# Performance work log

Measured on AMD Instinct MI355X. Metric: run time of the kernel, lower is better.

## Reference

```python
import jax, jax.numpy as jnp
import numpy as np

N, D, G = 16384, 2048, 4096  # points, vocab_size (feature dim), num_groups


def setup_inputs() -> dict:
    key = jax.random.key(0)
    kx, ke = jax.random.split(key)
    x = jax.random.normal(kx, (N, D), dtype=jnp.float32)
    # trunc_normal_ init for the codebook; plain normal is fine for a numeric reference
    emb = jax.random.truncated_normal(ke, -2.0, 2.0, (G, D), dtype=jnp.float32)
    return {"x": x, "emb": emb}


def reference(x, emb):
    x2 = jnp.sum(x * x, axis=-1, keepdims=True)          # [N, 1]
    e2 = jnp.sum(emb * emb, axis=-1)                     # [G]
    sq = x2 + e2[None, :] - 2.0 * (x @ emb.T)            # [N, G]
    dist = jnp.sqrt(jnp.maximum(sq, 0.0))
    return -dist
```

## Files before the change

kernel.cpp:

```cpp
#include <hip/hip_runtime.h>
#include <hip/hip_bf16.h>

#define NPTS 16384
#define DIM  2048
#define NGRP 4096
#define BK   32
#define NT   (DIM / BK)

typedef __bf16 bf16x8 __attribute__((ext_vector_type(8)));
typedef unsigned short u16x8 __attribute__((ext_vector_type(8)));
typedef float f32x4 __attribute__((ext_vector_type(4)));

__device__ __forceinline__ unsigned short f2bf(float f) {
  union { float f; unsigned u; } v; v.f = f;
  unsigned u = v.u;
  return (unsigned short)((u + 0x7FFFu + ((u >> 16) & 1u)) >> 16);
}
__device__ __forceinline__ float bflo(unsigned u) { return __uint_as_float(u << 16); }
__device__ __forceinline__ float bfhi(unsigned u) { return __uint_as_float(u & 0xffff0000u); }

__device__ __forceinline__ void gload16(const void* g, void* lds) {
  __builtin_amdgcn_global_load_lds(
      (const __attribute__((address_space(1))) unsigned*)g,
      (__attribute__((address_space(3))) unsigned*)lds, 16, 0, 0);
}

__device__ __forceinline__ bool sniff_bf16(const void* X) {
  const int lane = threadIdx.x & 63;
  unsigned hb = (((const unsigned short*)X)[lane] >> 8) & 0x7Fu;
  unsigned long long m = __ballot(hb >= 0x3Bu && hb <= 0x41u);
  return __popcll(m) >= 48;
}

__global__ __launch_bounds__(256) void prep_all_kernel(
    const void* __restrict__ Xin, const void* __restrict__ Ein,
    unsigned short* __restrict__ Xbf, unsigned short* __restrict__ Ebf,
    float* __restrict__ x2, float* __restrict__ e2) {
  const int lane  = threadIdx.x & 63;
  const int wavei = threadIdx.x >> 6;
  const bool isbf = sniff_bf16(Xin);

  const int grow = blockIdx.x * 4 + wavei;
  const void* in; unsigned short* q; float* nrm; int row;
  if (grow < NPTS) { in = Xin; q = Xbf; nrm = x2; row = grow; }
  else             { in = Ein; q = Ebf; nrm = e2; row = grow - NPTS; }

  float s = 0.f;
  if (isbf) {
    const unsigned short* p = (const unsigned short*)in + (size_t)row * DIM;
#pragma unroll
    for (int it = 0; it < 4; ++it) {
      uint4 v = *(const uint4*)(p + it * 512 + lane * 8);
      float f;
      f = bflo(v.x); s += f * f;  f = bfhi(v.x); s += f * f;
      f = bflo(v.y); s += f * f;  f = bfhi(v.y); s += f * f;
      f = bflo(v.z); s += f * f;  f = bfhi(v.z); s += f * f;
      f = bflo(v.w); s += f * f;  f = bfhi(v.w); s += f * f;
    }
  } else {
    const float* p = (const float*)in + (size_t)row * DIM;
    unsigned short* qq = q + (size_t)row * DIM;
#pragma unroll
    for (int it = 0; it < 4; ++it) {
      float4 a = *(const float4*)(p + it * 512 + lane * 8);
      float4 b = *(const float4*)(p + it * 512 + lane * 8 + 4);
      s += a.x * a.x + a.y * a.y + a.z * a.z + a.w * a.w;
      s += b.x * b.x + b.y * b.y + b.z * b.z + b.w * b.w;
      u16x8 r;
      r[0] = f2bf(a.x); r[1] = f2bf(a.y); r[2] = f2bf(a.z); r[3] = f2bf(a.w);
      r[4] = f2bf(b.x); r[5] = f2bf(b.y); r[6] = f2bf(b.z); r[7] = f2bf(b.w);
      *(u16x8*)(qq + it * 512 + lane * 8) = r;
    }
  }
#pragma unroll
  for (int off = 32; off > 0; off >>= 1) s += __shfl_down(s, off, 64);
  if (lane == 0) nrm[row] = s;
}

#define A_OFF 0
#define B_OFF 8192

__global__ __launch_bounds__(512, 2) void gemm_8p_kernel(
    const void* __restrict__ Xin, const unsigned short* __restrict__ Xws,
    const void* __restrict__ Ein, const unsigned short* __restrict__ Ews,
    const float* __restrict__ x2, const float* __restrict__ e2,
    void* __restrict__ outv) {
  __shared__ __align__(16) unsigned short sbuf[4][16384];

  const int tid  = threadIdx.x;
  const int lane = tid & 63;
  const int wave = tid >> 6;
  const int wm   = wave >> 2;
  const int wn   = wave & 3;
  const int quad = lane >> 4;
  const int l16  = lane & 15;

  const bool isbf = sniff_bf16(Xin);
  const unsigned short* X = isbf ? (const unsigned short*)Xin : Xws;
  const unsigned short* E = isbf ? (const unsigned short*)Ein : Ews;

  const int rowBase = blockIdx.y * 256;
  const int colBase = blockIdx.x * 256;

  const int srow = tid >> 2;
  const int scol = (tid & 3) * 8;
  const size_t gA = (size_t)(rowBase + srow) * DIM + scol;
  const size_t gB = (size_t)(colBase + srow) * DIM + scol;
  const size_t HSTRIDE = (size_t)128 * DIM;

  const int aoff = (wm * 128 + l16) * 32 + quad * 8;
  const int boff = B_OFF + (wn * 64 + l16) * 32 + quad * 8;

  f32x4 zero = {0.f, 0.f, 0.f, 0.f};
  f32x4 acc[8][4];
#pragma unroll
  for (int mt = 0; mt < 8; ++mt)
#pragma unroll
    for (int nt = 0; nt < 4; ++nt) acc[mt][nt] = zero;

#define STAGE_A(t_) do { const size_t k_ = (size_t)(t_) * BK;                         \
    gload16(X + gA + k_,           &sbuf[(t_) & 3][A_OFF + wave * 512]);              \
    gload16(X + gA + HSTRIDE + k_, &sbuf[(t_) & 3][A_OFF + 4096 + wave * 512]);       \
  } while (0)
#define STAGE_B(t_) do { const size_t k_ = (size_t)(t_) * BK;                         \
    gload16(E + gB + k_,           &sbuf[(t_) & 3][B_OFF + wave * 512]);              \
    gload16(E + gB + HSTRIDE + k_, &sbuf[(t_) & 3][B_OFF + 4096 + wave * 512]);       \
  } while (0)

#define TILE(t_, DOSTAGE_, VM_) do {                                                  \
    asm volatile("s_waitcnt vmcnt(" #VM_ ")" ::: "memory");                           \
    __builtin_amdgcn_s_barrier();                                                     \
    __builtin_amdgcn_sched_barrier(0);                                                \
    const unsigned short* sb_ = sbuf[(t_) & 3];                                       \
    bf16x8 aL_[4], aH_[4], bF_[4];                                                    \
    _Pragma("unroll") for (int mt = 0; mt < 4; ++mt)                                  \
      aL_[mt] = *(const bf16x8*)(const void*)(sb_ + aoff + mt * 512);                 \
    _Pragma("unroll") for (int nt = 0; nt < 4; ++nt)                                  \
      bF_[nt] = *(const bf16x8*)(const void*)(sb_ + boff + nt * 512);                 \
    if (DOSTAGE_) STAGE_A((t_) + 3);                                                  \
    __builtin_amdgcn_s_setprio(1);                                                    \
    _Pragma("unroll") for (int mt = 0; mt < 4; ++mt)                                  \
      _Pragma("unroll") for (int nt = 0; nt < 4; ++nt)                                \
        acc[mt][nt] = __builtin_amdgcn_mfma_f32_16x16x32_bf16(aL_[mt], bF_[nt],       \
                                                              acc[mt][nt], 0, 0, 0);  \
    __builtin_amdgcn_s_setprio(0);                                                    \
    asm volatile("" ::: "memory");                                                    \
    __builtin_amdgcn_s_barrier();                                                     \
    __builtin_amdgcn_sched_barrier(0);                                                \
    _Pragma("unroll") for (int mt = 0; mt < 4; ++mt)                                  \
      aH_[mt] = *(const bf16x8*)(const void*)(sb_ + aoff + (mt + 4) * 512);           \
    if (DOSTAGE_) STAGE_B((t_) + 3);                                                  \
    __builtin_amdgcn_s_setprio(1);                                                    \
    _Pragma("unroll") for (int mt = 0; mt < 4; ++mt)                                  \
      _Pragma("unroll") for (int nt = 0; nt < 4; ++nt)                                \
        acc[mt + 4][nt] = __builtin_amdgcn_mfma_f32_16x16x32_bf16(aH_[mt], bF_[nt],   \
                                                              acc[mt + 4][nt], 0, 0, 0); \
    __builtin_amdgcn_s_setprio(0);                                                    \
    asm volatile("" ::: "memory");                                                    \
    __builtin_amdgcn_s_barrier();                                                     \
    __builtin_amdgcn_sched_barrier(0);                                                \
  } while (0)

  STAGE_A(0); STAGE_B(0);
  STAGE_A(1); STAGE_B(1);
  STAGE_A(2); STAGE_B(2);

  for (int t = 0; t < NT - 3; ++t) {
    TILE(t, true, 8);
  }
  TILE(NT - 3, false, 8);
  TILE(NT - 2, false, 4);
  TILE(NT - 1, false, 0);
#undef TILE
#undef STAGE_A
#undef STAGE_B

  float ec[4];
#pragma unroll
  for (int nt = 0; nt < 4; ++nt) ec[nt] = e2[colBase + wn * 64 + nt * 16 + l16];

  if (isbf) {
    unsigned short* out = (unsigned short*)outv;
#pragma unroll
    for (int mt = 0; mt < 8; ++mt)
#pragma unroll
      for (int r = 0; r < 4; ++r) {
        const int row = rowBase + wm * 128 + mt * 16 + quad * 4 + r;
        const float xr = x2[row];
#pragma unroll
        for (int nt = 0; nt < 4; ++nt) {
          const int col = colBase + wn * 64 + nt * 16 + l16;
          float sq = xr + ec[nt] - 2.0f * acc[mt][nt][r];
          sq = sq > 0.f ? sq : 0.f;
          out[(size_t)row * NGRP + col] = f2bf(-__builtin_sqrtf(sq));
        }
      }
  } else {
    float* out = (float*)outv;
#pragma unroll
    for (int mt = 0; mt < 8; ++mt)
#pragma unroll
      for (int r = 0; r < 4; ++r) {
        const int row = rowBase + wm * 128 + mt * 16 + quad * 4 + r;
        const float xr = x2[row];
#pragma unroll
        for (int nt = 0; nt < 4; ++nt) {
          const int col = colBase + wn * 64 + nt * 16 + l16;
          float sq = xr + ec[nt] - 2.0f * acc[mt][nt][r];
          sq = sq > 0.f ? sq : 0.f;
          out[(size_t)row * NGRP + col] = -__builtin_sqrtf(sq);
        }
      }
  }
}


__global__ void sniff_kernel(const unsigned short* __restrict__ X, int* __restrict__ flag) {
  if (threadIdx.x == 0 && blockIdx.x == 0) {
    int c = 0;
    for (int i = 0; i < 64; ++i) {
      unsigned b = (X[i] >> 8) & 0x7F;
      c += (b >= 0x3B && b <= 0x41) ? 1 : 0;
    }
    *flag = (c >= 48) ? 1 : 0;
  }
}

__global__ __launch_bounds__(256) void rownorm_kernel(const void* __restrict__ in,
                                                      float* __restrict__ out,
                                                      const int* __restrict__ flag) {
  const int wave = threadIdx.x >> 6;
  const int lane = threadIdx.x & 63;
  const int row  = blockIdx.x * 4 + wave;
  float s = 0.f;
  if (*flag) {
    const unsigned short* p = (const unsigned short*)in + (size_t)row * DIM;
#pragma unroll
    for (int it = 0; it < 4; ++it) {
      uint4 v = *(const uint4*)(p + it * 512 + lane * 8);
      float f;
      f = bflo(v.x); s += f * f;  f = bfhi(v.x); s += f * f;
      f = bflo(v.y); s += f * f;  f = bfhi(v.y); s += f * f;
      f = bflo(v.z); s += f * f;  f = bfhi(v.z); s += f * f;
      f = bflo(v.w); s += f * f;  f = bfhi(v.w); s += f * f;
    }
  } else {
    const float* p = (const float*)in + (size_t)row * DIM;
#pragma unroll
    for (int it = 0; it < 4; ++it) {
      float4 a = *(const float4*)(p + it * 512 + lane * 8);
      float4 b = *(const float4*)(p + it * 512 + lane * 8 + 4);
      s += a.x * a.x + a.y * a.y + a.z * a.z + a.w * a.w;
      s += b.x * b.x + b.y * b.y + b.z * b.z + b.w * b.w;
    }
  }
#pragma unroll
  for (int off = 32; off > 0; off >>= 1) s += __shfl_down(s, off, 64);
  if (lane == 0) out[row] = s;
}

__device__ __forceinline__ u16x8 cvt8(const float* p) {
  float4 a = *(const float4*)p;
  float4 b = *(const float4*)(p + 4);
  u16x8 r;
  r[0] = f2bf(a.x); r[1] = f2bf(a.y); r[2] = f2bf(a.z); r[3] = f2bf(a.w);
  r[4] = f2bf(b.x); r[5] = f2bf(b.y); r[6] = f2bf(b.z); r[7] = f2bf(b.w);
  return r;
}

__global__ __launch_bounds__(256) void gemm_dist_kernel(
    const void* __restrict__ Xv, const void* __restrict__ Ev,
    const float* __restrict__ x2, const float* __restrict__ e2,
    void* __restrict__ outv, const int* __restrict__ flag) {
  __shared__ __align__(16) unsigned short sA[128 * 32];
  __shared__ __align__(16) unsigned short sB[128 * 32];

  const bool isbf = (*flag != 0);
  const int tid  = threadIdx.x;
  const int lane = tid & 63;
  const int wave = tid >> 6;
  const int wm   = wave >> 1;
  const int wn   = wave & 1;
  const int quad = lane >> 4;
  const int l16  = lane & 15;

  const int rowBase = blockIdx.y * 128;
  const int colBase = blockIdx.x * 128;

  const int flat0 = tid * 8;
  const int flat1 = (tid + 256) * 8;
  const int r0 = flat0 >> 5, c0 = flat0 & 31;
  const int r1 = flat1 >> 5, c1 = flat1 & 31;

  const size_t iA0 = (size_t)(rowBase + r0) * DIM + c0;
  const size_t iA1 = (size_t)(rowBase + r1) * DIM + c1;
  const size_t iB0 = (size_t)(colBase + r0) * DIM + c0;
  const size_t iB1 = (size_t)(colBase + r1) * DIM + c1;

  f32x4 zero = {0.f, 0.f, 0.f, 0.f};
  f32x4 acc[4][4];
#pragma unroll
  for (int mt = 0; mt < 4; ++mt)
#pragma unroll
    for (int nt = 0; nt < 4; ++nt) acc[mt][nt] = zero;

  for (int k0 = 0; k0 < DIM; k0 += 32) {
    if (isbf) {
      const unsigned short* X = (const unsigned short*)Xv;
      const unsigned short* E = (const unsigned short*)Ev;
      *(uint4*)(sA + flat0) = *(const uint4*)(X + iA0 + k0);
      *(uint4*)(sA + flat1) = *(const uint4*)(X + iA1 + k0);
      *(uint4*)(sB + flat0) = *(const uint4*)(E + iB0 + k0);
      *(uint4*)(sB + flat1) = *(const uint4*)(E + iB1 + k0);
    } else {
      const float* X = (const float*)Xv;
      const float* E = (const float*)Ev;
      *(u16x8*)(sA + flat0) = cvt8(X + iA0 + k0);
      *(u16x8*)(sA + flat1) = cvt8(X + iA1 + k0);
      *(u16x8*)(sB + flat0) = cvt8(E + iB0 + k0);
      *(u16x8*)(sB + flat1) = cvt8(E + iB1 + k0);
    }
    __syncthreads();

    bf16x8 a[4], b[4];
#pragma unroll
    for (int mt = 0; mt < 4; ++mt)
      a[mt] = *(const bf16x8*)(const void*)(sA + (wm * 64 + mt * 16 + l16) * 32 + quad * 8);
#pragma unroll
    for (int nt = 0; nt < 4; ++nt)
      b[nt] = *(const bf16x8*)(const void*)(sB + (wn * 64 + nt * 16 + l16) * 32 + quad * 8);
#pragma unroll
    for (int mt = 0; mt < 4; ++mt)
#pragma unroll
      for (int nt = 0; nt < 4; ++nt)
        acc[mt][nt] = __builtin_amdgcn_mfma_f32_16x16x32_bf16(a[mt], b[nt], acc[mt][nt], 0, 0, 0);
    __syncthreads();
  }

  float ec[4];
#pragma unroll
  for (int nt = 0; nt < 4; ++nt) ec[nt] = e2[colBase + wn * 64 + nt * 16 + l16];

  if (isbf) {
    unsigned short* out = (unsigned short*)outv;
#pragma unroll
    for (int mt = 0; mt < 4; ++mt)
#pragma unroll
      for (int r = 0; r < 4; ++r) {
        const int row = rowBase + wm * 64 + mt * 16 + quad * 4 + r;
        const float xr = x2[row];
#pragma unroll
        for (int nt = 0; nt < 4; ++nt) {
          const int col = colBase + wn * 64 + nt * 16 + l16;
          float sq = xr + ec[nt] - 2.0f * acc[mt][nt][r];
          sq = sq > 0.f ? sq : 0.f;
          out[(size_t)row * NGRP + col] = f2bf(-__builtin_sqrtf(sq));
        }
      }
  } else {
    float* out = (float*)outv;
#pragma unroll
    for (int mt = 0; mt < 4; ++mt)
#pragma unroll
      for (int r = 0; r < 4; ++r) {
        const int row = rowBase + wm * 64 + mt * 16 + quad * 4 + r;
        const float xr = x2[row];
#pragma unroll
        for (int nt = 0; nt < 4; ++nt) {
          const int col = colBase + wn * 64 + nt * 16 + l16;
          float sq = xr + ec[nt] - 2.0f * acc[mt][nt][r];
          sq = sq > 0.f ? sq : 0.f;
          out[(size_t)row * NGRP + col] = -__builtin_sqrtf(sq);
        }
      }
  }
}

extern "C" void kernel_launch(void* const* d_in, const int* in_sizes, int n_in,
                              void* d_out, int out_size, void* d_ws, size_t ws_size,
                              hipStream_t stream) {
  const size_t xbf = (size_t)NPTS * DIM;
  const size_t ebf = (size_t)NGRP * DIM;
  const size_t need = (xbf + ebf) * sizeof(unsigned short)
                    + (NPTS + NGRP) * sizeof(float) + 64;

  if (ws_size >= need) {
    unsigned short* Xbf = (unsigned short*)d_ws;
    unsigned short* Ebf = Xbf + xbf;
    float* x2 = (float*)(Ebf + ebf);
    float* e2 = x2 + NPTS;

    prep_all_kernel<<<(NPTS + NGRP) / 4, 256, 0, stream>>>(d_in[0], d_in[1],
                                                           Xbf, Ebf, x2, e2);
    dim3 grid(NGRP / 256, NPTS / 256);
    gemm_8p_kernel<<<grid, 512, 0, stream>>>(d_in[0], Xbf, d_in[1], Ebf,
                                             x2, e2, d_out);
  } else {
    float* x2 = (float*)d_ws;
    float* e2 = x2 + NPTS;
    int* flag = (int*)(e2 + NGRP);

    sniff_kernel<<<1, 64, 0, stream>>>((const unsigned short*)d_in[0], flag);
    rownorm_kernel<<<NPTS / 4, 256, 0, stream>>>(d_in[0], x2, flag);
    rownorm_kernel<<<NGRP / 4, 256, 0, stream>>>(d_in[1], e2, flag);
    dim3 grid(NGRP / 128, NPTS / 128);
    gemm_dist_kernel<<<grid, 256, 0, stream>>>(d_in[0], d_in[1], x2, e2, d_out, flag);
  }
}
```

Before: 634.0 us.

## Software-pipeline LDS fragment reads across K tiles to overlap with MFMA

Restructures the main GEMM loop so the A-low and B fragments for the next K tile are read from LDS at the end of the current tile, and the A-high reads are issued before the first MFMA block. Global prefetch stages are reordered, and vmcnt waits move to the end of each tile so LDS latency overlaps matrix math. The loop is also marked unroll 1 to keep code size small. This raises register pressure because fragments stay live across iterations, and the barrier and wait placement must stay correct for the 4-buffer ring.

Measured after the change: 626.6 us. No clear change (-1.2%).

```diff
diff --git a/kernel.cpp b/kernel.cpp
--- a/kernel.cpp
+++ b/kernel.cpp
@@ -118,6 +118,8 @@
 #pragma unroll
     for (int nt = 0; nt < 4; ++nt) acc[mt][nt] = zero;
 
+  bf16x8 aL[4], aH[4], bF[4];
+
 #define STAGE_A(t_) do { const size_t k_ = (size_t)(t_) * BK;                         \
     gload16(X + gA + k_,           &sbuf[(t_) & 3][A_OFF + wave * 512]);              \
     gload16(X + gA + HSTRIDE + k_, &sbuf[(t_) & 3][A_OFF + 4096 + wave * 512]);       \
@@ -127,51 +129,64 @@
     gload16(E + gB + HSTRIDE + k_, &sbuf[(t_) & 3][B_OFF + 4096 + wave * 512]);       \
   } while (0)
 
-#define TILE(t_, DOSTAGE_, VM_) do {                                                  \
-    asm volatile("s_waitcnt vmcnt(" #VM_ ")" ::: "memory");                           \
-    __builtin_amdgcn_s_barrier();                                                     \
+#define DSR_L(t_) do { const unsigned short* sb_ = sbuf[(t_) & 3];                    \
+    _Pragma("unroll") for (int mt = 0; mt < 4; ++mt)                                  \
+      aL[mt] = *(const bf16x8*)(const void*)(sb_ + aoff + mt * 512);                  \
+    _Pragma("unroll") for (int nt = 0; nt < 4; ++nt)                                  \
+      bF[nt] = *(const bf16x8*)(const void*)(sb_ + boff + nt * 512);                  \
+  } while (0)
+#define DSR_H(t_) do { const unsigned short* sb_ = sbuf[(t_) & 3];                    \
+    _Pragma("unroll") for (int mt = 0; mt < 4; ++mt)                                  \
+      aH[mt] = *(const bf16x8*)(const void*)(sb_ + aoff + (mt + 4) * 512);            \
+  } while (0)
+
+#define BODY(t_, DOSTAGE_, VMN_, DONEXT_) do {                                        \
+    if (DOSTAGE_) STAGE_A((t_) + 3);                                                  \
+    asm volatile("s_waitcnt lgkmcnt(0)" ::: "memory");                                \
     __builtin_amdgcn_sched_barrier(0);                                                \
-    const unsigned short* sb_ = sbuf[(t_) & 3];                                       \
-    bf16x8 aL_[4], aH_[4], bF_[4];                                                    \
-    _Pragma("unroll") for (int mt = 0; mt < 4; ++mt)                                  \
-      aL_[mt] = *(const bf16x8*)(const void*)(sb_ + aoff + mt * 512);                 \
-    _Pragma("unroll") for (int nt = 0; nt < 4; ++nt)                                  \
-      bF_[nt] = *(const bf16x8*)(const void*)(sb_ + boff + nt * 512);                 \
-    if (DOSTAGE_) STAGE_A((t_) + 3);                                                  \
+    DSR_H(t_);                                                                        \
+    __builtin_amdgcn_sched_barrier(0);                                                \
     __builtin_amdgcn_s_setprio(1);                                                    \
     _Pragma("unroll") for (int mt = 0; mt < 4; ++mt)                                  \
       _Pragma("unroll") for (int nt = 0; nt < 4; ++nt)                                \
-        acc[mt][nt] = __builtin_amdgcn_mfma_f32_16x16x32_bf16(aL_[mt], bF_[nt],       \
+        acc[mt][nt] = __builtin_amdgcn_mfma_f32_16x16x32_bf16(aL[mt], bF[nt],         \
                                                               acc[mt][nt], 0, 0, 0);  \
     __builtin_amdgcn_s_setprio(0);                                                    \
-    asm volatile("" ::: "memory");                                                    \
+    if (DOSTAGE_) STAGE_B((t_) + 3);                                                  \
     __builtin_amdgcn_s_barrier();                                                     \
+    asm volatile("s_waitcnt lgkmcnt(0)" ::: "memory");                                \
     __builtin_amdgcn_sched_barrier(0);                                                \
-    _Pragma("unroll") for (int mt = 0; mt < 4; ++mt)                                  \
-      aH_[mt] = *(const bf16x8*)(const void*)(sb_ + aoff + (mt + 4) * 512);           \
-    if (DOSTAGE_) STAGE_B((t_) + 3);                                                  \
     __builtin_amdgcn_s_setprio(1);                                                    \
     _Pragma("unroll") for (int mt = 0; mt < 4; ++mt)                                  \
       _Pragma("unroll") for (int nt = 0; nt < 4; ++nt)                                \
-        acc[mt + 4][nt] = __builtin_amdgcn_mfma_f32_16x16x32_bf16(aH_[mt], bF_[nt],   \
+        acc[mt + 4][nt] = __builtin_amdgcn_mfma_f32_16x16x32_bf16(aH[mt], bF[nt],     \
                                                               acc[mt + 4][nt], 0, 0, 0); \
     __builtin_amdgcn_s_setprio(0);                                                    \
-    asm volatile("" ::: "memory");                                                    \
+    asm volatile("s_waitcnt vmcnt(" #VMN_ ")" ::: "memory");                          \
     __builtin_amdgcn_s_barrier();                                                     \
     __builtin_amdgcn_sched_barrier(0);                                                \
+    if (DONEXT_) { DSR_L((t_) + 1); __builtin_amdgcn_sched_barrier(0); }              \
   } while (0)
 
   STAGE_A(0); STAGE_B(0);
   STAGE_A(1); STAGE_B(1);
   STAGE_A(2); STAGE_B(2);
-
+  asm volatile("s_waitcnt vmcnt(8)" ::: "memory");
+  __builtin_amdgcn_s_barrier();
+  __builtin_amdgcn_sched_barrier(0);
+  DSR_L(0);
+  __builtin_amdgcn_sched_barrier(0);
+
+#pragma unroll 1
   for (int t = 0; t < NT - 3; ++t) {
-    TILE(t, true, 8);
-  }
-  TILE(NT - 3, false, 8);
-  TILE(NT - 2, false, 4);
-  TILE(NT - 1, false, 0);
-#undef TILE
+    BODY(t, true, 8, true);
+  }
+  BODY(NT - 3, false, 4, true);
+  BODY(NT - 2, false, 0, true);
+  BODY(NT - 1, false, 0, false);
+#undef BODY
+#undef DSR_L
+#undef DSR_H
 #undef STAGE_A
 #undef STAGE_B
 
@@ -184,13 +199,13 @@
 #pragma unroll
     for (int mt = 0; mt < 8; ++mt)
 #pragma unroll
-      for (int r = 0; r < 4; ++r) {
-        const int row = rowBase + wm * 128 + mt * 16 + quad * 4 + r;
+      for (int r2 = 0; r2 < 4; ++r2) {
+        const int row = rowBase + wm * 128 + mt * 16 + quad * 4 + r2;
         const float xr = x2[row];
 #pragma unroll
         for (int nt = 0; nt < 4; ++nt) {
           const int col = colBase + wn * 64 + nt * 16 + l16;
-          float sq = xr + ec[nt] - 2.0f * acc[mt][nt][r];
+          float sq = xr + ec[nt] - 2.0f * acc[mt][nt][r2];
           sq = sq > 0.f ? sq : 0.f;
           out[(size_t)row * NGRP + col] = f2bf(-__builtin_sqrtf(sq));
         }
@@ -200,13 +215,13 @@
 #pragma unroll
     for (int mt = 0; mt < 8; ++mt)
 #pragma unroll
-      for (int r = 0; r < 4; ++r) {
-        const int row = rowBase + wm * 128 + mt * 16 + quad * 4 + r;
+      for (int r2 = 0; r2 < 4; ++r2) {
+        const int row = rowBase + wm * 128 + mt * 16 + quad * 4 + r2;
         const float xr = x2[row];
 #pragma unroll
         for (int nt = 0; nt < 4; ++nt) {
           const int col = colBase + wn * 64 + nt * 16 + l16;
-          float sq = xr + ec[nt] - 2.0f * acc[mt][nt][r];
+          float sq = xr + ec[nt] - 2.0f * acc[mt][nt][r2];
           sq = sq > 0.f ? sq : 0.f;
           out[(size_t)row * NGRP + col] = -__builtin_sqrtf(sq);
         }
```

## Switch GEMM to 32x32x16 MFMA with BK=64 double buffering and XOR-swizzled LDS

Applied to the files above, without the earlier changes.

Replaces the 16x16x32 MFMA tiling with 32x32x16 bf16 MFMAs, which cuts the LDS fragment reads needed per FLOP. The K tile grows to 64 with two LDS buffers instead of four buffers of K=32, and the shared-memory layout is XOR-swizzled to avoid bank conflicts on the wider rows. The pipeline interleaves LDS reads for alternating k-substeps with MFMA groups. The cost is a shallower prefetch depth (two stages instead of three) and larger accumulator fragments, which may add register pressure at two blocks per CU.

Result: no change. 642.4 us (+1.3%).

```diff
diff --git a/kernel.cpp b/kernel.cpp
--- a/kernel.cpp
+++ b/kernel.cpp
@@ -4,12 +4,13 @@
 #define NPTS 16384
 #define DIM  2048
 #define NGRP 4096
-#define BK   32
-#define NT   (DIM / BK)
+#define BK2  64
+#define NT2  (DIM / BK2)
 
 typedef __bf16 bf16x8 __attribute__((ext_vector_type(8)));
 typedef unsigned short u16x8 __attribute__((ext_vector_type(8)));
 typedef float f32x4 __attribute__((ext_vector_type(4)));
+typedef float f32x16 __attribute__((ext_vector_type(16)));
 
 __device__ __forceinline__ unsigned short f2bf(float f) {
   union { float f; unsigned u; } v; v.f = f;
@@ -77,23 +78,20 @@
   if (lane == 0) nrm[row] = s;
 }
 
-#define A_OFF 0
-#define B_OFF 8192
-
-__global__ __launch_bounds__(512, 2) void gemm_8p_kernel(
+__global__ __launch_bounds__(512, 2) void gemm_32_kernel(
     const void* __restrict__ Xin, const unsigned short* __restrict__ Xws,
     const void* __restrict__ Ein, const unsigned short* __restrict__ Ews,
     const float* __restrict__ x2, const float* __restrict__ e2,
     void* __restrict__ outv) {
-  __shared__ __align__(16) unsigned short sbuf[4][16384];
+  __shared__ __align__(16) unsigned short sbuf[2][32768];
 
   const int tid  = threadIdx.x;
   const int lane = tid & 63;
   const int wave = tid >> 6;
   const int wm   = wave >> 2;
   const int wn   = wave & 3;
-  const int quad = lane >> 4;
-  const int l16  = lane & 15;
+  const int l31  = lane & 31;
+  const int hi   = lane >> 5;
 
   const bool isbf = sniff_bf16(Xin);
   const unsigned short* X = isbf ? (const unsigned short*)Xin : Xws;
@@ -102,95 +100,103 @@
   const int rowBase = blockIdx.y * 256;
   const int colBase = blockIdx.x * 256;
 
-  const int srow = tid >> 2;
-  const int scol = (tid & 3) * 8;
-  const size_t gA = (size_t)(rowBase + srow) * DIM + scol;
-  const size_t gB = (size_t)(colBase + srow) * DIM + scol;
-  const size_t HSTRIDE = (size_t)128 * DIM;
-
-  const int aoff = (wm * 128 + l16) * 32 + quad * 8;
-  const int boff = B_OFF + (wn * 64 + l16) * 32 + quad * 8;
-
-  f32x4 zero = {0.f, 0.f, 0.f, 0.f};
-  f32x4 acc[8][4];
-#pragma unroll
-  for (int mt = 0; mt < 8; ++mt)
-#pragma unroll
-    for (int nt = 0; nt < 4; ++nt) acc[mt][nt] = zero;
-
-#define STAGE_A(t_) do { const size_t k_ = (size_t)(t_) * BK;                         \
-    gload16(X + gA + k_,           &sbuf[(t_) & 3][A_OFF + wave * 512]);              \
-    gload16(X + gA + HSTRIDE + k_, &sbuf[(t_) & 3][A_OFF + 4096 + wave * 512]);       \
+  const int srow  = tid >> 3;
+  const int scol8 = ((tid & 7) ^ (srow & 7)) * 8;
+  size_t gAo[4], gBo[4];
+#pragma unroll
+  for (int g = 0; g < 4; ++g) {
+    gAo[g] = (size_t)(rowBase + g * 64 + srow) * DIM + scol8;
+    gBo[g] = (size_t)(colBase + g * 64 + srow) * DIM + scol8;
+  }
+
+  const int arow = wm * 128 + l31;
+  const int brow = wn * 64 + l31;
+  const int axor = (l31 & 7) << 4;
+
+  f32x16 acc[4][2];
+#pragma unroll
+  for (int m = 0; m < 4; ++m)
+#pragma unroll
+    for (int n = 0; n < 2; ++n)
+#pragma unroll
+      for (int r = 0; r < 16; ++r) acc[m][n][r] = 0.f;
+
+  bf16x8 aE[4], bE[2], aO[4], bO[2];
+
+#define STAGE(t_) do { unsigned short* sb_ = sbuf[(t_) & 1];                   \
+    const size_t kk_ = (size_t)(t_) * BK2;                                     \
+    _Pragma("unroll") for (int g = 0; g < 4; ++g)                              \
+      gload16(X + gAo[g] + kk_, sb_ + g * 4096 + wave * 512);                  \
+    _Pragma("unroll") for (int g = 0; g < 4; ++g)                              \
+      gload16(E + gBo[g] + kk_, sb_ + 16384 + g * 4096 + wave * 512);          \
   } while (0)
-#define STAGE_B(t_) do { const size_t k_ = (size_t)(t_) * BK;                         \
-    gload16(E + gB + k_,           &sbuf[(t_) & 3][B_OFF + wave * 512]);              \
-    gload16(E + gB + HSTRIDE + k_, &sbuf[(t_) & 3][B_OFF + 4096 + wave * 512]);       \
+
+#define DSR(t_, ks_, A_, B_) do {                                              \
+    const char* sa_ = (const char*)sbuf[(t_) & 1];                             \
+    const char* sbb_ = sa_ + 32768;                                            \
+    const int kx_ = ((ks_) * 32 + hi * 16) ^ axor;                             \
+    _Pragma("unroll") for (int m = 0; m < 4; ++m)                              \
+      A_[m] = *(const bf16x8*)(const void*)(sa_ + (arow + m * 32) * 128 + kx_);\
+    _Pragma("unroll") for (int n = 0; n < 2; ++n)                              \
+      B_[n] = *(const bf16x8*)(const void*)(sbb_ + (brow + n * 32) * 128 + kx_);\
   } while (0)
 
-#define TILE(t_, DOSTAGE_, VM_) do {                                                  \
-    asm volatile("s_waitcnt vmcnt(" #VM_ ")" ::: "memory");                           \
-    __builtin_amdgcn_s_barrier();                                                     \
-    __builtin_amdgcn_sched_barrier(0);                                                \
-    const unsigned short* sb_ = sbuf[(t_) & 3];                                       \
-    bf16x8 aL_[4], aH_[4], bF_[4];                                                    \
-    _Pragma("unroll") for (int mt = 0; mt < 4; ++mt)                                  \
-      aL_[mt] = *(const bf16x8*)(const void*)(sb_ + aoff + mt * 512);                 \
-    _Pragma("unroll") for (int nt = 0; nt < 4; ++nt)                                  \
-      bF_[nt] = *(const bf16x8*)(const void*)(sb_ + boff + nt * 512);                 \
-    if (DOSTAGE_) STAGE_A((t_) + 3);                                                  \
-    __builtin_amdgcn_s_setprio(1);                                                    \
-    _Pragma("unroll") for (int mt = 0; mt < 4; ++mt)                                  \
-      _Pragma("unroll") for (int nt = 0; nt < 4; ++nt)                                \
-        acc[mt][nt] = __builtin_amdgcn_mfma_f32_16x16x32_bf16(aL_[mt], bF_[nt],       \
-                                                              acc[mt][nt], 0, 0, 0);  \
-    __builtin_amdgcn_s_setprio(0);                                                    \
-    asm volatile("" ::: "memory");                                                    \
-    __builtin_amdgcn_s_barrier();                                                     \
-    __builtin_amdgcn_sched_barrier(0);                                                \
-    _Pragma("unroll") for (int mt = 0; mt < 4; ++mt)                                  \
-      aH_[mt] = *(const bf16x8*)(const void*)(sb_ + aoff + (mt + 4) * 512);           \
-    if (DOSTAGE_) STAGE_B((t_) + 3);                                                  \
-    __builtin_amdgcn_s_setprio(1);                                                    \
-    _Pragma("unroll") for (int mt = 0; mt < 4; ++mt)                                  \
-      _Pragma("unroll") for (int nt = 0; nt < 4; ++nt)                                \
-        acc[mt + 4][nt] = __builtin_amdgcn_mfma_f32_16x16x32_bf16(aH_[mt], bF_[nt],   \
-                                                              acc[mt + 4][nt], 0, 0, 0); \
-    __builtin_amdgcn_s_setprio(0);                                                    \
-    asm volatile("" ::: "memory");                                                    \
-    __builtin_amdgcn_s_barrier();                                                     \
-    __builtin_amdgcn_sched_barrier(0);                                                \
+#define MFMA8(A_, B_) do {                                                     \
+    __builtin_amdgcn_s_setprio(1);                                             \
+    _Pragma("unroll") for (int m = 0; m < 4; ++m)                              \
+      _Pragma("unroll") for (int n = 0; n < 2; ++n)                            \
+        acc[m][n] = __builtin_amdgcn_mfma_f32_32x32x16_bf16(A_[m], B_[n],      \
+                                                            acc[m][n], 0, 0, 0); \
+    __builtin_amdgcn_s_setprio(0);                                             \
   } while (0)
 
-  STAGE_A(0); STAGE_B(0);
-  STAGE_A(1); STAGE_B(1);
-  STAGE_A(2); STAGE_B(2);
-
-  for (int t = 0; t < NT - 3; ++t) {
-    TILE(t, true, 8);
-  }
-  TILE(NT - 3, false, 8);
-  TILE(NT - 2, false, 4);
-  TILE(NT - 1, false, 0);
-#undef TILE
-#undef STAGE_A
-#undef STAGE_B
-
-  float ec[4];
-#pragma unroll
-  for (int nt = 0; nt < 4; ++nt) ec[nt] = e2[colBase + wn * 64 + nt * 16 + l16];
+#define BODY(t_, DOSTAGE_, VMS_) do {                                          \
+    asm volatile("s_waitcnt vmcnt(" VMS_ ")" ::: "memory");                    \
+    __builtin_amdgcn_s_barrier();                                              \
+    __builtin_amdgcn_sched_barrier(0);                                         \
+    DSR(t_, 0, aE, bE);                                                        \
+    DSR(t_, 1, aO, bO);                                                        \
+    MFMA8(aE, bE);                                                    \
+    DSR(t_, 2, aE, bE);                                                        \
+    MFMA8(aO, bO);                                                    \
+    DSR(t_, 3, aO, bO);                                                        \
+    MFMA8(aE, bE);                                                    \
+    MFMA8(aO, bO);                                                    \
+    asm volatile("" ::: "memory");                                             \
+    __builtin_amdgcn_s_barrier();                                              \
+    __builtin_amdgcn_sched_barrier(0);                                         \
+    if (DOSTAGE_) STAGE((t_) + 2);                                             \
+  } while (0)
+
+  STAGE(0); STAGE(1);
+
+#pragma unroll 1
+  for (int t = 0; t < NT2 - 2; ++t) {
+    BODY(t, true, "8");
+  }
+  BODY(NT2 - 2, false, "8");
+  BODY(NT2 - 1, false, "0");
+#undef BODY
+#undef MFMA8
+#undef DSR
+#undef STAGE
+
+  float ec[2];
+#pragma unroll
+  for (int n = 0; n < 2; ++n) ec[n] = e2[colBase + wn * 64 + n * 32 + l31];
 
   if (isbf) {
     unsigned short* out = (unsigned short*)outv;
 #pragma unroll
-    for (int mt = 0; mt < 8; ++mt)
-#pragma unroll
-      for (int r = 0; r < 4; ++r) {
-        const int row = rowBase + wm * 128 + mt * 16 + quad * 4 + r;
+    for (int m = 0; m < 4; ++m)
+#pragma unroll
+      for (int r = 0; r < 16; ++r) {
+        const int row = rowBase + wm * 128 + m * 32 + (r & 3) + 8 * (r >> 2) + 4 * hi;
         const float xr = x2[row];
 #pragma unroll
-        for (int nt = 0; nt < 4; ++nt) {
-          const int col = colBase + wn * 64 + nt * 16 + l16;
-          float sq = xr + ec[nt] - 2.0f * acc[mt][nt][r];
+        for (int n = 0; n < 2; ++n) {
+          const int col = colBase + wn * 64 + n * 32 + l31;
+          float sq = xr + ec[n] - 2.0f * acc[m][n][r];
           sq = sq > 0.f ? sq : 0.f;
           out[(size_t)row * NGRP + col] = f2bf(-__builtin_sqrtf(sq));
         }
@@ -198,15 +204,15 @@
   } else {
     float* out = (float*)outv;
 #pragma unroll
-    for (int mt = 0; mt < 8; ++mt)
-#pragma unroll
-      for (int r = 0; r < 4; ++r) {
-        const int row = rowBase + wm * 128 + mt * 16 + quad * 4 + r;
+    for (int m = 0; m < 4; ++m)
+#pragma unroll
+      for (int r = 0; r < 16; ++r) {
+        const int row = rowBase + wm * 128 + m * 32 + (r & 3) + 8 * (r >> 2) + 4 * hi;
         const float xr = x2[row];
 #pragma unroll
-        for (int nt = 0; nt < 4; ++nt) {
-          const int col = colBase + wn * 64 + nt * 16 + l16;
-          float sq = xr + ec[nt] - 2.0f * acc[mt][nt][r];
+        for (int n = 0; n < 2; ++n) {
+          const int col = colBase + wn * 64 + n * 32 + l31;
+          float sq = xr + ec[n] - 2.0f * acc[m][n][r];
           sq = sq > 0.f ? sq : 0.f;
           out[(size_t)row * NGRP + col] = -__builtin_sqrtf(sq);
         }
@@ -393,7 +399,7 @@
     prep_all_kernel<<<(NPTS + NGRP) / 4, 256, 0, stream>>>(d_in[0], d_in[1],
                                                            Xbf, Ebf, x2, e2);
     dim3 grid(NGRP / 256, NPTS / 256);
-    gemm_8p_kernel<<<grid, 512, 0, stream>>>(d_in[0], Xbf, d_in[1], Ebf,
+    gemm_32_kernel<<<grid, 512, 0, stream>>>(d_in[0], Xbf, d_in[1], Ebf,
                                              x2, e2, d_out);
   } else {
     float* x2 = (float*)d_ws;
```
